# Kernel tuning notes

Hardware: AMD Instinct MI355X
Metric: run time of the kernel (lower is better)

Reference implementation:

```python
import jax, jax.numpy as jnp
import numpy as np

PULSE_THRESHOLD = 0.01
REAL_W = 1.0
IMAG_W = 1.0
INT_W = 1.0
PHASE_W = 1.0
MSE_W_SUM = REAL_W + IMAG_W + INT_W + PHASE_W


def _hilbert_batch(x):
    # x: [B, N] real. Replicates the module's hilbert(): zero lower half of
    # spectrum, double upper half (N even: bin N/2 kept at 1).
    N = x.shape[-1]
    idx = jnp.arange(N)
    if N % 2 == 0:
        H = jnp.where(idx == N // 2, 1.0, jnp.where(idx > N // 2, 2.0, 0.0))
    else:
        H = jnp.where(idx >= (N + 1) // 2, 2.0, 0.0)
    Xf = jnp.fft.fft(x, axis=-1)
    return jnp.fft.ifft(Xf * H.astype(Xf.dtype), axis=-1)


def _first_last(mask):
    # mask: bool [N]; fallback (0, N-1) when empty, matching torch.nonzero min/max path
    N = mask.shape[0]
    any_m = jnp.any(mask)
    first = jnp.where(any_m, jnp.argmax(mask), 0)
    last = jnp.where(any_m, N - 1 - jnp.argmax(mask[::-1]), N - 1)
    return first, last


def setup_inputs() -> dict:
    key = jax.random.key(0)
    k1, k2, k3, k4 = jax.random.split(key, 4)
    B, N = 512, 8192
    return {
        "prediction": jax.random.normal(k1, (B, N), dtype=jnp.float32),
        "label": jax.random.normal(k2, (B, 2 * N), dtype=jnp.float32),
        "spectrogram": jax.random.uniform(k3, (B, 1, 64, 64), dtype=jnp.float32),
        "header": jax.random.uniform(k4, (B, 5), dtype=jnp.float32),
    }


def reference(prediction, label, spectrogram, header):
    B, N = prediction.shape  # N == half_size
    ana = _hilbert_batch(prediction)              # [B, N] complex64
    pred_real, pred_imag = ana.real, ana.imag
    lab_real = label[:, :N]
    lab_imag = label[:, N:]

    lab_int = lab_real ** 2 + lab_imag ** 2
    pred_int = pred_real ** 2 + pred_imag ** 2
    lab_phase = jnp.arctan2(lab_imag, lab_real)
    pred_phase = jnp.arctan2(pred_imag, pred_real)

    # per-sample significant-region bounds (min of real/imag firsts, max of lasts)
    fr, lr = jax.vmap(_first_last)(jnp.abs(lab_real) > PULSE_THRESHOLD)
    fi, li = jax.vmap(_first_last)(jnp.abs(lab_imag) > PULSE_THRESHOLD)
    first = jnp.minimum(fr, fi)
    last = jnp.maximum(lr, li)
    pos = jnp.arange(N)
    # phase_mask[first:last] = 1 (end-exclusive, as in the torch code)
    phase_mask = ((pos[None, :] >= first[:, None]) & (pos[None, :] < last[:, None])).astype(prediction.dtype)

    mse_real = jnp.mean((pred_real - lab_real) ** 2, axis=-1) * REAL_W
    mse_imag = jnp.mean((pred_imag - lab_imag) ** 2, axis=-1) * IMAG_W
    mse_int = jnp.mean((pred_int - lab_int) ** 2, axis=-1) * INT_W
    mse_phase = jnp.mean(((pred_phase - lab_phase) ** 2) * phase_mask, axis=-1) * PHASE_W
    mse_per = (mse_real + mse_imag + mse_int + mse_phase) / MSE_W_SUM  # [B]

    # The torch loop never resets mse_loss, so sample j contributes (B - j) times.
    coef = (B - jnp.arange(B)).astype(mse_per.dtype)
    loss = jnp.sum(coef * mse_per) / B
    return loss
```

## Files before the change

kernel.cpp:

```cpp
#include <hip/hip_runtime.h>

#define NROWS   512
#define THREADS 512
#define PULSE_THR 0.01f

typedef float2 cpx;

__device__ __forceinline__ cpx cadd(cpx a, cpx b){ return make_float2(a.x+b.x, a.y+b.y); }
__device__ __forceinline__ cpx csub(cpx a, cpx b){ return make_float2(a.x-b.x, a.y-b.y); }
__device__ __forceinline__ cpx cmul(cpx a, cpx b){
    return make_float2(fmaf(a.x, b.x, -(a.y*b.y)), fmaf(a.x, b.y, a.y*b.x));
}
__device__ __forceinline__ cpx cmuli(cpx a){ return make_float2(-a.y, a.x); }
__device__ __forceinline__ cpx twf(float rev){
    return make_float2(__builtin_amdgcn_cosf(rev), __builtin_amdgcn_sinf(rev));
}
__device__ __forceinline__ int slotf(int e){ return e ^ ((e >> 4) & 15) ^ ((e >> 8) & 15); }
__device__ __forceinline__ int rev3(int t){ return ((t & 7) << 6) | (t & 0x38) | (t >> 6); }

__device__ __forceinline__ float fast_atan2(float y, float x){
    float ax = fabsf(x), ay = fabsf(y);
    float mx = fmaxf(ax, ay), mn = fminf(ax, ay);
    float a  = mn * __builtin_amdgcn_rcpf(mx);
    if (mx == 0.0f) a = 0.0f;
    float s = a * a;
    float p = fmaf(s, fmaf(s, fmaf(s, fmaf(s, 0.0208351f, -0.085133f),
                                   0.180141f), -0.3302995f), 0.9998660f);
    p = p * a;
    if (ay > ax)   p = 1.57079632679f - p;
    if (x < 0.0f)  p = 3.14159265359f - p;
    return (y < 0.0f) ? -p : p;
}

__device__ __forceinline__ void twiddle7(float sj_L, cpx* w){
    w[0] = twf(sj_L);
    w[1] = twf(2.0f * sj_L);
    w[3] = twf(4.0f * sj_L);
    w[2] = cmul(w[0], w[1]);
    w[4] = cmul(w[0], w[3]);
    w[5] = cmul(w[1], w[3]);
    w[6] = cmul(w[2], w[3]);
}

__device__ __forceinline__ void dft8_fwd(cpx* x){
    const float S = 0.70710678118654752f;
    cpx a0=cadd(x[0],x[4]), a1=cadd(x[1],x[5]), a2=cadd(x[2],x[6]), a3=cadd(x[3],x[7]);
    cpx b0=csub(x[0],x[4]), b1=csub(x[1],x[5]), b2=csub(x[2],x[6]), b3=csub(x[3],x[7]);
    cpx c0=cadd(a0,a2), c1=csub(a0,a2), c2=cadd(a1,a3), c3=csub(a1,a3);
    x[0]=cadd(c0,c2);
    x[4]=csub(c0,c2);
    x[2]=csub(c1,cmuli(c3));
    x[6]=cadd(c1,cmuli(c3));
    cpx t1 = make_float2(S*(b1.x+b1.y), S*(b1.y-b1.x));
    cpx t2 = make_float2(b2.y, -b2.x);
    cpx t3 = make_float2(S*(b3.y-b3.x), -S*(b3.x+b3.y));
    cpx d0=cadd(b0,t2), d1=csub(b0,t2), d2=cadd(t1,t3), d3=csub(t1,t3);
    x[1]=cadd(d0,d2);
    x[5]=csub(d0,d2);
    x[3]=csub(d1,cmuli(d3));
    x[7]=cadd(d1,cmuli(d3));
}
__device__ __forceinline__ void dft8_inv(cpx* x){
    const float S = 0.70710678118654752f;
    cpx a0=cadd(x[0],x[4]), a1=cadd(x[1],x[5]), a2=cadd(x[2],x[6]), a3=cadd(x[3],x[7]);
    cpx b0=csub(x[0],x[4]), b1=csub(x[1],x[5]), b2=csub(x[2],x[6]), b3=csub(x[3],x[7]);
    cpx c0=cadd(a0,a2), c1=csub(a0,a2), c2=cadd(a1,a3), c3=csub(a1,a3);
    x[0]=cadd(c0,c2);
    x[4]=csub(c0,c2);
    x[2]=cadd(c1,cmuli(c3));
    x[6]=csub(c1,cmuli(c3));
    cpx t1 = make_float2(S*(b1.x-b1.y), S*(b1.y+b1.x));
    cpx t2 = make_float2(-b2.y, b2.x);
    cpx t3 = make_float2(-S*(b3.x+b3.y), S*(b3.x-b3.y));
    cpx d0=cadd(b0,t2), d1=csub(b0,t2), d2=cadd(t1,t3), d3=csub(t1,t3);
    x[1]=cadd(d0,d2);
    x[5]=csub(d0,d2);
    x[3]=cadd(d1,cmuli(d3));
    x[7]=csub(d1,cmuli(d3));
}

template<int L>
__device__ __forceinline__ void fwd_stage8(cpx* sd, int tid){
    constexpr int q = L / 8;
    const int j    = tid & (q - 1);
    const int base = ((tid & ~(q - 1)) << 3) + j;
    cpx v[8];
    #pragma unroll
    for (int m = 0; m < 8; ++m) v[m] = sd[slotf(base + m*q)];
    cpx w[7];
    twiddle7(-(float)j * (1.0f/(float)L), w);
    dft8_fwd(v);
    #pragma unroll
    for (int m = 1; m < 8; ++m) v[m] = cmul(v[m], w[m-1]);
    #pragma unroll
    for (int m = 0; m < 8; ++m) sd[slotf(base + m*q)] = v[m];
}
template<int L>
__device__ __forceinline__ void inv_stage8(cpx* sd, int tid){
    constexpr int q = L / 8;
    const int j    = tid & (q - 1);
    const int base = ((tid & ~(q - 1)) << 3) + j;
    cpx v[8];
    #pragma unroll
    for (int m = 0; m < 8; ++m) v[m] = sd[slotf(base + m*q)];
    cpx w[7];
    twiddle7((float)j * (1.0f/(float)L), w);
    #pragma unroll
    for (int m = 1; m < 8; ++m) v[m] = cmul(v[m], w[m-1]);
    dft8_inv(v);
    #pragma unroll
    for (int m = 0; m < 8; ++m) sd[slotf(base + m*q)] = v[m];
}

__global__ __launch_bounds__(THREADS, 4) void pulse_row_kernel(
    const float* __restrict__ pred,
    const float* __restrict__ label,
    float* __restrict__ mse_per)
{
    __shared__ cpx   sdat[4096];
    __shared__ int   sred[8][4];
    __shared__ float swsum[8];
    __shared__ int   s_first, s_last;
    __shared__ float s_mean;

    const int row  = blockIdx.x;
    const int tid  = threadIdx.x;
    const int lane = tid & 63;
    const int wid  = tid >> 6;

    const float* lab_r = label + (size_t)row * 16384;
    const float* lab_i = lab_r + 8192;

    int minr = 8192, maxr = -1, mini = 8192, maxi = -1;
    const float4* lr4 = (const float4*)lab_r;
    const float4* li4 = (const float4*)lab_i;
    #pragma unroll
    for (int it = 0; it < 4; ++it){
        int idx = tid + THREADS * it;
        float4 a = lr4[idx];
        float4 b = li4[idx];
        int n0 = idx << 2;
        if (fabsf(a.x) > PULSE_THR){ minr = min(minr, n0);   maxr = max(maxr, n0);   }
        if (fabsf(a.y) > PULSE_THR){ minr = min(minr, n0+1); maxr = max(maxr, n0+1); }
        if (fabsf(a.z) > PULSE_THR){ minr = min(minr, n0+2); maxr = max(maxr, n0+2); }
        if (fabsf(a.w) > PULSE_THR){ minr = min(minr, n0+3); maxr = max(maxr, n0+3); }
        if (fabsf(b.x) > PULSE_THR){ mini = min(mini, n0);   maxi = max(maxi, n0);   }
        if (fabsf(b.y) > PULSE_THR){ mini = min(mini, n0+1); maxi = max(maxi, n0+1); }
        if (fabsf(b.z) > PULSE_THR){ mini = min(mini, n0+2); maxi = max(maxi, n0+2); }
        if (fabsf(b.w) > PULSE_THR){ mini = min(mini, n0+3); maxi = max(maxi, n0+3); }
    }
    #pragma unroll
    for (int off = 32; off; off >>= 1){
        minr = min(minr, __shfl_down(minr, off));
        maxr = max(maxr, __shfl_down(maxr, off));
        mini = min(mini, __shfl_down(mini, off));
        maxi = max(maxi, __shfl_down(maxi, off));
    }
    if (lane == 0){ sred[wid][0]=minr; sred[wid][1]=maxr; sred[wid][2]=mini; sred[wid][3]=maxi; }

    const float2* zin = (const float2*)(pred + (size_t)row * 8192);
    cpx zv[8];
    #pragma unroll
    for (int u = 0; u < 8; ++u) zv[u] = zin[tid + THREADS * u];
    {
        cpx v[8];
        #pragma unroll
        for (int m = 0; m < 8; ++m) v[m] = zv[m];
        cpx w[7];
        twiddle7(-(float)tid * (1.0f/4096.0f), w);
        dft8_fwd(v);
        #pragma unroll
        for (int m = 1; m < 8; ++m) v[m] = cmul(v[m], w[m-1]);
        #pragma unroll
        for (int m = 0; m < 8; ++m) sdat[slotf(tid + 512*m)] = v[m];
    }
    __syncthreads();

    if (tid == 0){
        int a = 8192, b = -1, c = 8192, d = -1;
        for (int w = 0; w < 8; ++w){
            a = min(a, sred[w][0]); b = max(b, sred[w][1]);
            c = min(c, sred[w][2]); d = max(d, sred[w][3]);
        }
        int fr  = (a == 8192) ? 0 : a;
        int lr_ = (b < 0) ? 8191 : b;
        int fi  = (c == 8192) ? 0 : c;
        int li_ = (d < 0) ? 8191 : d;
        s_first = min(fr, fi);
        s_last  = max(lr_, li_);
    }

    fwd_stage8<512>(sdat, tid); __syncthreads();
    fwd_stage8<64 >(sdat, tid); __syncthreads();

    {
        const int s  = rev3(tid);
        const int sp = (512 - s) & 511;
        const int tp = rev3(sp);
        cpx va[8], vb[8];
        #pragma unroll
        for (int a = 0; a < 8; ++a) va[a] = sdat[slotf(8*tid + a)];
        #pragma unroll
        for (int a = 0; a < 8; ++a) vb[a] = sdat[slotf(8*tp  + a)];
        __syncthreads();
        dft8_fwd(va);
        dft8_fwd(vb);
        if (tid == 0){
            s_mean = (va[0].x + va[0].y) * (1.0f/8192.0f);
            #pragma unroll
            for (int i = 0; i < 8; ++i) vb[i] = va[(i + 1) & 7];
        }
        cpx es = twf((float)s * (1.0f/8192.0f));
        const float W16c[8] = {1.f, 0.92387953251f, 0.70710678119f, 0.38268343236f,
                               0.f, -0.38268343236f, -0.70710678119f, -0.92387953251f};
        const float W16s[8] = {0.f, 0.38268343236f, 0.70710678119f, 0.92387953251f,
                               1.f, 0.92387953251f, 0.70710678119f, 0.38268343236f};
        cpx C[8];
        #pragma unroll
        for (int a = 0; a < 8; ++a){
            cpx w  = cmul(make_float2(W16c[a], W16s[a]), es);
            cpx wc = make_float2(w.x, -w.y);
            cpx Zb = vb[7 - a];
            cpx E  = make_float2(0.5f*(va[a].x + Zb.x), 0.5f*(va[a].y - Zb.y));
            cpx D  = make_float2(0.5f*(va[a].x - Zb.x), 0.5f*(va[a].y + Zb.y));
            C[a] = csub(cmul(wc, D), cmul(w, E));
        }
        if (tid == 0) C[0] = make_float2(0.f, 0.f);
        dft8_inv(C);
        #pragma unroll
        for (int a = 0; a < 8; ++a) sdat[slotf(8*tid + a)] = C[a];
    }
    __syncthreads();

    inv_stage8<64 >(sdat, tid); __syncthreads();
    inv_stage8<512>(sdat, tid); __syncthreads();

    const int   first = s_first;
    const int   last  = s_last;
    const float mean  = s_mean;
    const float invM  = 1.0f/4096.0f;
    const float2* lr2 = (const float2*)lab_r;
    const float2* li2 = (const float2*)lab_i;

    float2 lrv[8], liv[8];
    #pragma unroll
    for (int m = 0; m < 8; ++m){
        lrv[m] = lr2[tid + 512*m];
        liv[m] = li2[tid + 512*m];
    }

    float acc = 0.f;
    cpx y[8];
    {
        #pragma unroll
        for (int m = 0; m < 8; ++m) y[m] = sdat[slotf(tid + 512*m)];
        cpx w[7];
        twiddle7((float)tid * (1.0f/4096.0f), w);
        #pragma unroll
        for (int m = 1; m < 8; ++m) y[m] = cmul(y[m], w[m-1]);
        dft8_inv(y);
    }
    #pragma unroll
    for (int m = 0; m < 8; ++m){
        int tt = tid + 512*m;
        float pi0 = y[m].x * invM, pi1 = y[m].y * invM;
        float pr0 = zv[m].x - mean, pr1 = zv[m].y - mean;
        int n = 2 * tt;
        {
            float dr = pr0 - lrv[m].x, di = pi0 - liv[m].x;
            acc = fmaf(dr, dr, acc);
            acc = fmaf(di, di, acc);
            float dint = fmaf(pr0, pr0, pi0*pi0) - fmaf(lrv[m].x, lrv[m].x, liv[m].x*liv[m].x);
            acc = fmaf(dint, dint, acc);
            if (n >= first && n < last){
                float dph = fast_atan2(pi0, pr0) - fast_atan2(liv[m].x, lrv[m].x);
                acc = fmaf(dph, dph, acc);
            }
        }
        {
            float dr = pr1 - lrv[m].y, di = pi1 - liv[m].y;
            acc = fmaf(dr, dr, acc);
            acc = fmaf(di, di, acc);
            float dint = fmaf(pr1, pr1, pi1*pi1) - fmaf(lrv[m].y, lrv[m].y, liv[m].y*liv[m].y);
            acc = fmaf(dint, dint, acc);
            if (n + 1 >= first && n + 1 < last){
                float dph = fast_atan2(pi1, pr1) - fast_atan2(liv[m].y, lrv[m].y);
                acc = fmaf(dph, dph, acc);
            }
        }
    }
    #pragma unroll
    for (int off = 32; off; off >>= 1) acc += __shfl_down(acc, off);
    if (lane == 0) swsum[wid] = acc;
    __syncthreads();
    if (tid == 0){
        float t = 0.f;
        for (int w = 0; w < 8; ++w) t += swsum[w];
        mse_per[row] = t * (1.0f/8192.0f) * 0.25f;
    }
}

__global__ __launch_bounds__(512) void pulse_final_kernel(
    const float* __restrict__ mse_per, float* __restrict__ out)
{
    const int tid = threadIdx.x;
    double v = 0.0;
    if (tid < NROWS) v = (double)(NROWS - tid) * (double)mse_per[tid];
    #pragma unroll
    for (int off = 32; off; off >>= 1) v += __shfl_down(v, off);
    __shared__ double lds[8];
    const int lane = tid & 63, wid = tid >> 6;
    if (lane == 0) lds[wid] = v;
    __syncthreads();
    if (tid == 0){
        double t = 0.0;
        for (int i = 0; i < 8; ++i) t += lds[i];
        out[0] = (float)(t / (double)NROWS);
    }
}

extern "C" void kernel_launch(void* const* d_in, const int* in_sizes, int n_in,
                              void* d_out, int out_size, void* d_ws, size_t ws_size,
                              hipStream_t stream) {
    const float* pred  = (const float*)d_in[0];
    const float* label = (const float*)d_in[1];
    float* mse_per = (float*)d_ws;
    float* out     = (float*)d_out;

    pulse_row_kernel<<<NROWS, THREADS, 0, stream>>>(pred, label, mse_per);
    pulse_final_kernel<<<1, 512, 0, stream>>>(mse_per, out);
}
```

Measured before the change: 27.59 us.

## Fuse threshold scan into loss pass and replace final kernel with atomics

Removes the separate initial read of the label rows for the significant-region scan and instead computes the first/last bounds from the label values already loaded for the loss computation. Phase errors are computed for every element and kept in registers, then masked once the block-wide bounds are known. The second reduction kernel is replaced by a per-block float atomicAdd into the output after a memset. This trades duplicated global label reads and a kernel launch for extra atan2 work on every element, an extra barrier, more register pressure, and nondeterministic float summation order.

```diff
diff --git a/kernel.cpp b/kernel.cpp
--- a/kernel.cpp
+++ b/kernel.cpp
@@ -115,7 +115,7 @@
 __global__ __launch_bounds__(THREADS, 4) void pulse_row_kernel(
     const float* __restrict__ pred,
     const float* __restrict__ label,
-    float* __restrict__ mse_per)
+    float* __restrict__ out)
 {
     __shared__ cpx   sdat[4096];
     __shared__ int   sred[8][4];
@@ -131,33 +131,6 @@
     const float* lab_r = label + (size_t)row * 16384;
     const float* lab_i = lab_r + 8192;
 
-    int minr = 8192, maxr = -1, mini = 8192, maxi = -1;
-    const float4* lr4 = (const float4*)lab_r;
-    const float4* li4 = (const float4*)lab_i;
-    #pragma unroll
-    for (int it = 0; it < 4; ++it){
-        int idx = tid + THREADS * it;
-        float4 a = lr4[idx];
-        float4 b = li4[idx];
-        int n0 = idx << 2;
-        if (fabsf(a.x) > PULSE_THR){ minr = min(minr, n0);   maxr = max(maxr, n0);   }
-        if (fabsf(a.y) > PULSE_THR){ minr = min(minr, n0+1); maxr = max(maxr, n0+1); }
-        if (fabsf(a.z) > PULSE_THR){ minr = min(minr, n0+2); maxr = max(maxr, n0+2); }
-        if (fabsf(a.w) > PULSE_THR){ minr = min(minr, n0+3); maxr = max(maxr, n0+3); }
-        if (fabsf(b.x) > PULSE_THR){ mini = min(mini, n0);   maxi = max(maxi, n0);   }
-        if (fabsf(b.y) > PULSE_THR){ mini = min(mini, n0+1); maxi = max(maxi, n0+1); }
-        if (fabsf(b.z) > PULSE_THR){ mini = min(mini, n0+2); maxi = max(maxi, n0+2); }
-        if (fabsf(b.w) > PULSE_THR){ mini = min(mini, n0+3); maxi = max(maxi, n0+3); }
-    }
-    #pragma unroll
-    for (int off = 32; off; off >>= 1){
-        minr = min(minr, __shfl_down(minr, off));
-        maxr = max(maxr, __shfl_down(maxr, off));
-        mini = min(mini, __shfl_down(mini, off));
-        maxi = max(maxi, __shfl_down(maxi, off));
-    }
-    if (lane == 0){ sred[wid][0]=minr; sred[wid][1]=maxr; sred[wid][2]=mini; sred[wid][3]=maxi; }
-
     const float2* zin = (const float2*)(pred + (size_t)row * 8192);
     cpx zv[8];
     #pragma unroll
@@ -175,20 +148,6 @@
         for (int m = 0; m < 8; ++m) sdat[slotf(tid + 512*m)] = v[m];
     }
     __syncthreads();
-
-    if (tid == 0){
-        int a = 8192, b = -1, c = 8192, d = -1;
-        for (int w = 0; w < 8; ++w){
-            a = min(a, sred[w][0]); b = max(b, sred[w][1]);
-            c = min(c, sred[w][2]); d = max(d, sred[w][3]);
-        }
-        int fr  = (a == 8192) ? 0 : a;
-        int lr_ = (b < 0) ? 8191 : b;
-        int fi  = (c == 8192) ? 0 : c;
-        int li_ = (d < 0) ? 8191 : d;
-        s_first = min(fr, fi);
-        s_last  = max(lr_, li_);
-    }
 
     fwd_stage8<512>(sdat, tid); __syncthreads();
     fwd_stage8<64 >(sdat, tid); __syncthreads();
@@ -235,9 +194,6 @@
     inv_stage8<64 >(sdat, tid); __syncthreads();
     inv_stage8<512>(sdat, tid); __syncthreads();
 
-    const int   first = s_first;
-    const int   last  = s_last;
-    const float mean  = s_mean;
     const float invM  = 1.0f/4096.0f;
     const float2* lr2 = (const float2*)lab_r;
     const float2* li2 = (const float2*)lab_i;
@@ -249,7 +205,6 @@
         liv[m] = li2[tid + 512*m];
     }
 
-    float acc = 0.f;
     cpx y[8];
     {
         #pragma unroll
@@ -260,35 +215,75 @@
         for (int m = 1; m < 8; ++m) y[m] = cmul(y[m], w[m-1]);
         dft8_inv(y);
     }
+
+    const float mean = s_mean;
+    float acc = 0.f;
+    float ph[16];
+    int minr = 8192, maxr = -1, mini = 8192, maxi = -1;
     #pragma unroll
     for (int m = 0; m < 8; ++m){
-        int tt = tid + 512*m;
+        int n = 2 * (tid + 512*m);
         float pi0 = y[m].x * invM, pi1 = y[m].y * invM;
         float pr0 = zv[m].x - mean, pr1 = zv[m].y - mean;
-        int n = 2 * tt;
+        float lr0 = lrv[m].x, li0 = liv[m].x;
+        float lr1 = lrv[m].y, li1 = liv[m].y;
         {
-            float dr = pr0 - lrv[m].x, di = pi0 - liv[m].x;
+            float dr = pr0 - lr0, di = pi0 - li0;
             acc = fmaf(dr, dr, acc);
             acc = fmaf(di, di, acc);
-            float dint = fmaf(pr0, pr0, pi0*pi0) - fmaf(lrv[m].x, lrv[m].x, liv[m].x*liv[m].x);
+            float dint = fmaf(pr0, pr0, pi0*pi0) - fmaf(lr0, lr0, li0*li0);
             acc = fmaf(dint, dint, acc);
-            if (n >= first && n < last){
-                float dph = fast_atan2(pi0, pr0) - fast_atan2(liv[m].x, lrv[m].x);
-                acc = fmaf(dph, dph, acc);
-            }
+            float dph = fast_atan2(pi0, pr0) - fast_atan2(li0, lr0);
+            ph[2*m] = dph * dph;
+            if (fabsf(lr0) > PULSE_THR){ minr = min(minr, n); maxr = max(maxr, n); }
+            if (fabsf(li0) > PULSE_THR){ mini = min(mini, n); maxi = max(maxi, n); }
         }
         {
-            float dr = pr1 - lrv[m].y, di = pi1 - liv[m].y;
+            float dr = pr1 - lr1, di = pi1 - li1;
             acc = fmaf(dr, dr, acc);
             acc = fmaf(di, di, acc);
-            float dint = fmaf(pr1, pr1, pi1*pi1) - fmaf(lrv[m].y, lrv[m].y, liv[m].y*liv[m].y);
+            float dint = fmaf(pr1, pr1, pi1*pi1) - fmaf(lr1, lr1, li1*li1);
             acc = fmaf(dint, dint, acc);
-            if (n + 1 >= first && n + 1 < last){
-                float dph = fast_atan2(pi1, pr1) - fast_atan2(liv[m].y, lrv[m].y);
-                acc = fmaf(dph, dph, acc);
-            }
-        }
-    }
+            float dph = fast_atan2(pi1, pr1) - fast_atan2(li1, lr1);
+            ph[2*m+1] = dph * dph;
+            if (fabsf(lr1) > PULSE_THR){ minr = min(minr, n+1); maxr = max(maxr, n+1); }
+            if (fabsf(li1) > PULSE_THR){ mini = min(mini, n+1); maxi = max(maxi, n+1); }
+        }
+    }
+
+    #pragma unroll
+    for (int off = 32; off; off >>= 1){
+        minr = min(minr, __shfl_down(minr, off));
+        maxr = max(maxr, __shfl_down(maxr, off));
+        mini = min(mini, __shfl_down(mini, off));
+        maxi = max(maxi, __shfl_down(maxi, off));
+    }
+    if (lane == 0){ sred[wid][0]=minr; sred[wid][1]=maxr; sred[wid][2]=mini; sred[wid][3]=maxi; }
+    __syncthreads();
+    if (tid == 0){
+        int a = 8192, b = -1, c = 8192, d = -1;
+        for (int w = 0; w < 8; ++w){
+            a = min(a, sred[w][0]); b = max(b, sred[w][1]);
+            c = min(c, sred[w][2]); d = max(d, sred[w][3]);
+        }
+        int fr  = (a == 8192) ? 0 : a;
+        int lr_ = (b < 0) ? 8191 : b;
+        int fi  = (c == 8192) ? 0 : c;
+        int li_ = (d < 0) ? 8191 : d;
+        s_first = min(fr, fi);
+        s_last  = max(lr_, li_);
+    }
+    __syncthreads();
+    const int first = s_first;
+    const int last  = s_last;
+
+    #pragma unroll
+    for (int m = 0; m < 8; ++m){
+        int n = 2 * (tid + 512*m);
+        if (n     >= first && n     < last) acc += ph[2*m];
+        if (n + 1 >= first && n + 1 < last) acc += ph[2*m+1];
+    }
+
     #pragma unroll
     for (int off = 32; off; off >>= 1) acc += __shfl_down(acc, off);
     if (lane == 0) swsum[wid] = acc;
@@ -296,26 +291,9 @@
     if (tid == 0){
         float t = 0.f;
         for (int w = 0; w < 8; ++w) t += swsum[w];
-        mse_per[row] = t * (1.0f/8192.0f) * 0.25f;
-    }
-}
-
-__global__ __launch_bounds__(512) void pulse_final_kernel(
-    const float* __restrict__ mse_per, float* __restrict__ out)
-{
-    const int tid = threadIdx.x;
-    double v = 0.0;
-    if (tid < NROWS) v = (double)(NROWS - tid) * (double)mse_per[tid];
-    #pragma unroll
-    for (int off = 32; off; off >>= 1) v += __shfl_down(v, off);
-    __shared__ double lds[8];
-    const int lane = tid & 63, wid = tid >> 6;
-    if (lane == 0) lds[wid] = v;
-    __syncthreads();
-    if (tid == 0){
-        double t = 0.0;
-        for (int i = 0; i < 8; ++i) t += lds[i];
-        out[0] = (float)(t / (double)NROWS);
+        float mse = t * (1.0f/8192.0f) * 0.25f;
+        float coef = (float)(NROWS - row);
+        atomicAdd(out, coef * mse * (1.0f/(float)NROWS));
     }
 }
 
@@ -324,9 +302,8 @@
                               hipStream_t stream) {
     const float* pred  = (const float*)d_in[0];
     const float* label = (const float*)d_in[1];
-    float* mse_per = (float*)d_ws;
-    float* out     = (float*)d_out;
-
-    pulse_row_kernel<<<NROWS, THREADS, 0, stream>>>(pred, label, mse_per);
-    pulse_final_kernel<<<1, 512, 0, stream>>>(mse_per, out);
-}
+    float* out = (float*)d_out;
+
+    hipMemsetAsync(out, 0, sizeof(float), stream);
+    pulse_row_kernel<<<NROWS, THREADS, 0, stream>>>(pred, label, out);
+}
```

Result: slower. 34.93 us (+26.6%).
